# Kernel optimization log

Hardware: AMD Instinct MI355X
Metric: run time of the kernel (lower is better)

The kernel has to match this reference:

```python
import jax, jax.numpy as jnp
import numpy as np

B, V_IN, V_OUT, C_IN, C_OUT, K, NNZ = 16, 1024, 4096, 128, 256, 18, 16384

def setup_inputs() -> dict:
    key = jax.random.key(0)
    ks = jax.random.split(key, 10)
    def lin(k, fan_in, fan_out):
        s = 1.0 / np.sqrt(fan_in)
        return jax.random.normal(k, (fan_in, fan_out), jnp.float32) * s
    return {
        "x": jax.random.normal(ks[0], (B, V_IN, C_IN), jnp.float32),
        "vals": jax.random.uniform(ks[1], (NNZ,), jnp.float32),
        "W1": lin(ks[2], 1 * C_IN, C_OUT),
        "b1": jnp.zeros((C_OUT,), jnp.float32),
        "Wd3": lin(ks[3], (K // 3) * C_IN, C_OUT // 4),
        "bd3": jnp.zeros((C_OUT // 4,), jnp.float32),
        "W2d3": lin(ks[4], (K // 3 * 2) * C_IN, C_OUT // 4),
        "b2d3": jnp.zeros((C_OUT // 4,), jnp.float32),
        "Wf": lin(ks[5], K * C_IN, C_OUT // 2),
        "bf": jnp.zeros((C_OUT // 2,), jnp.float32),
        "rows": jax.random.randint(ks[6], (NNZ,), 0, V_OUT, jnp.int32),
        "cols": jax.random.randint(ks[7], (NNZ,), 0, V_IN, jnp.int32),
        "spiral_idx": jax.random.randint(ks[8], (V_OUT, K), 0, V_OUT, jnp.int32),
    }

def _pool(x, rows, cols, vals, dim_size):
    # sparse upsample: gather cols, scale, scatter-add to rows
    gathered = x[:, cols, :] * vals[None, :, None]  # [B, nnz, C]
    return jnp.zeros((x.shape[0], dim_size, x.shape[2]), x.dtype).at[:, rows, :].add(gathered)

def _spiral_conv(feat, idx, W, b):
    # gather fixed spiral neighborhoods then shared linear layer
    Bz, V, C = feat.shape[0], idx.shape[0], feat.shape[2]
    g = feat[:, idx.reshape(-1), :].reshape(Bz, V, idx.shape[1] * C)  # [B, V, K*C]
    return g @ W + b

def reference(x, vals, W1, b1, Wd3, bd3, W2d3, b2d3, Wf, bf, rows, cols, spiral_idx):
    out = _pool(x, rows, cols, vals, V_OUT)  # [B, V_OUT, C_IN]
    k = spiral_idx.shape[1]
    short_cut = _spiral_conv(out, spiral_idx[:, :1], W1, b1)
    p_d3 = _spiral_conv(out, spiral_idx[:, : k // 3], Wd3, bd3)
    p_2d3 = _spiral_conv(out, spiral_idx[:, : k // 3 * 2], W2d3, b2d3)
    p = _spiral_conv(out, spiral_idx, Wf, bf)
    f = jnp.concatenate((p, p_2d3, p_d3), axis=2)  # [B, V_OUT, C_OUT]
    return jax.nn.relu(short_cut + f)
```

## Files before the change

### kernel.cpp

```cpp
#include <hip/hip_runtime.h>
#include <hip/hip_bf16.h>

#define B_SZ   16
#define V_IN   1024
#define V_OUT  4096
#define C_IN   128
#define C_OUT  256
#define K_NB   18
#define NNZ    16384
#define K_GEMM (K_NB * C_IN)
#define BK     64
#define NKT    (K_GEMM / BK)

typedef __attribute__((ext_vector_type(8))) short bf16x8;
typedef __attribute__((ext_vector_type(4))) float f32x4;

#define GLOAD16(src, dst) __builtin_amdgcn_global_load_lds( \
    (const __attribute__((address_space(1))) unsigned int*)(src), \
    (__attribute__((address_space(3))) unsigned int*)(dst), 16, 0, 0)

#define MFMA16(a_, b_, c_) __builtin_amdgcn_mfma_f32_16x16x32_bf16((a_), (b_), (c_), 0, 0, 0)

__global__ __launch_bounds__(1024) void csr_kernel(const int* __restrict__ rows,
                                                   int* __restrict__ offsets,
                                                   int* __restrict__ perm) {
    __shared__ int cnt[V_OUT];
    __shared__ int wsum[16];
    const int t = threadIdx.x;
    const int lane = t & 63, wid = t >> 6;
#pragma unroll
    for (int i = t; i < V_OUT; i += 1024) cnt[i] = 0;
    __syncthreads();
#pragma unroll
    for (int n = t; n < NNZ; n += 1024) atomicAdd(&cnt[rows[n]], 1);
    __syncthreads();
    const int base4 = t * 4;
    int c0 = cnt[base4], c1 = cnt[base4 + 1], c2 = cnt[base4 + 2], c3 = cnt[base4 + 3];
    int tot = c0 + c1 + c2 + c3;
    int v = tot;
#pragma unroll
    for (int d = 1; d < 64; d <<= 1) {
        int u = __shfl_up(v, d);
        if (lane >= d) v += u;
    }
    if (lane == 63) wsum[wid] = v;
    __syncthreads();
    int wbase = 0;
#pragma unroll
    for (int w = 0; w < 16; ++w) wbase += (w < wid) ? wsum[w] : 0;
    int incl = wbase + v;
    int excl = incl - tot;
    offsets[base4]     = excl;
    offsets[base4 + 1] = excl + c0;
    offsets[base4 + 2] = excl + c0 + c1;
    offsets[base4 + 3] = excl + c0 + c1 + c2;
    if (t == 1023) offsets[V_OUT] = incl;
    __syncthreads();
    cnt[base4]     = excl;
    cnt[base4 + 1] = excl + c0;
    cnt[base4 + 2] = excl + c0 + c1;
    cnt[base4 + 3] = excl + c0 + c1 + c2;
    __syncthreads();
#pragma unroll
    for (int n = t; n < NNZ; n += 1024) {
        int pos = atomicAdd(&cnt[rows[n]], 1);
        perm[pos] = n;
    }
}

__global__ __launch_bounds__(512) void pool_kernel(
    const float* __restrict__ x, const float* __restrict__ vals,
    const int* __restrict__ cols, const int* __restrict__ offsets,
    const int* __restrict__ perm, __hip_bfloat16* __restrict__ pool) {
    int r = blockIdx.x;
    int t = threadIdx.x;
    int b = t >> 5, c4 = t & 31;
    int j0 = offsets[r], j1 = offsets[r + 1];
    const float4* xb = (const float4*)x + (size_t)b * (V_IN * 32);
    float4 acc = {0.f, 0.f, 0.f, 0.f};
    for (int j = j0; j < j1; ++j) {
        int n = perm[j];
        float v = vals[n];
        float4 xv = xb[cols[n] * 32 + c4];
        acc.x += v * xv.x; acc.y += v * xv.y; acc.z += v * xv.z; acc.w += v * xv.w;
    }
    ushort4 o;
    o.x = __builtin_bit_cast(unsigned short, __float2bfloat16(acc.x));
    o.y = __builtin_bit_cast(unsigned short, __float2bfloat16(acc.y));
    o.z = __builtin_bit_cast(unsigned short, __float2bfloat16(acc.z));
    o.w = __builtin_bit_cast(unsigned short, __float2bfloat16(acc.w));
    ((ushort4*)pool)[((size_t)b * V_OUT + r) * 32 + c4] = o;
}

__global__ __launch_bounds__(256) void wcomb_kernel(
    const float* __restrict__ W1, const float* __restrict__ Wd3,
    const float* __restrict__ W2d3, const float* __restrict__ Wf,
    const float* __restrict__ b1, const float* __restrict__ bd3,
    const float* __restrict__ b2d3, const float* __restrict__ bf,
    __hip_bfloat16* __restrict__ wTs, float* __restrict__ bias) {
    const int blk = blockIdx.x;
    const int t   = threadIdx.x;
    if (blk == NKT * 4) {
        float v = b1[t];
        if (t < 128)      v += bf[t];
        else if (t < 192) v += b2d3[t - 128];
        else              v += bd3[t - 192];
        bias[t] = v;
        return;
    }
    const int kt = blk >> 2, part = blk & 3;
    __shared__ __hip_bfloat16 img[4096];
    const int k0 = kt * 64;

    auto put = [&](int cl, int col7, int kl, float v) {
        int kb    = (kl >> 3) << 4;
        int kslot = kb ^ (col7 << 4);
        int idx   = (((cl << 3) | (kslot >> 4)) << 3) | (kl & 7);
        img[idx] = __float2bfloat16(v);
    };

    if (part < 2) {
        const int cbase = part << 6;
        for (int i = t; i < 4096; i += 256) {
            int kl = i >> 6, cl = i & 63;
            int col = cbase + cl, r = k0 + kl;
            float v = Wf[r * 128 + col];
            if (r < 128) v += W1[r * 256 + col];
            put(cl, col & 7, kl, v);
        }
    } else if (part == 2) {
        for (int i = t; i < 4096; i += 256) {
            int kl = i >> 6, cl = i & 63;
            int r = k0 + kl;
            float v = (r < 1536) ? W2d3[r * 64 + cl] : 0.f;
            if (r < 128) v += W1[r * 256 + 128 + cl];
            put(cl, cl & 7, kl, v);
        }
    } else {
        for (int i = t; i < 4096; i += 256) {
            int kl = i >> 6, cl = i & 63;
            int r = k0 + kl;
            float v = (r < 768) ? Wd3[r * 64 + cl] : 0.f;
            if (r < 128) v += W1[r * 256 + 192 + cl];
            put(cl, cl & 7, kl, v);
        }
    }
    __syncthreads();
    ulonglong2* dst = (ulonglong2*)(wTs + (size_t)kt * 16384 + part * 4096);
    const ulonglong2* srcv = (const ulonglong2*)img;
#pragma unroll
    for (int i = t; i < 512; i += 256) dst[i] = srcv[i];
}

__global__ __launch_bounds__(1024, 4) void gemm_kernel(
    const __hip_bfloat16* __restrict__ pool,
    const __hip_bfloat16* __restrict__ wTs,
    const float* __restrict__ bias,
    const int* __restrict__ spiral,
    float* __restrict__ out)
{
    __shared__ __align__(16) char smem[149504];
    int* spl = (int*)(smem + 131072);

    const int tid  = threadIdx.x;
    const int lane = tid & 63;
    const int wid  = tid >> 6;
    const int wc   = wid & 3;
    const int wm   = (wid >> 2) << 6;

    const int bid = blockIdx.x;
    const int bm  = ((bid & 7) << 5) + (bid >> 3);
    const int b   = bm >> 4;
    const int v0  = (bm & 15) << 8;

    for (int i = tid; i < 256 * K_NB; i += 1024) {
        int j = i >> 8, row = i & 255;
        spl[i] = spiral[(v0 + row) * K_NB + j];
    }
    asm volatile("s_waitcnt vmcnt(0) lgkmcnt(0)" ::: "memory");
    __builtin_amdgcn_s_barrier();

    const char* poolBytes = (const char*)(pool + (size_t)b * V_OUT * C_IN);
    const char* wTsBytes  = (const char*)wTs;
    const int sb = ((tid & 7) << 4) ^ (((tid >> 3) & 7) << 4);

    auto stageA = [&](int kt) {
        const int j   = kt >> 1;
        const int c0b = (kt & 1) << 7;
        char* dst = smem + ((kt & 1) << 15);
#pragma unroll
        for (int ch = 0; ch < 2; ++ch) {
            int flat = (ch << 10) + tid;
            int sidx = spl[(j << 8) + (flat >> 3)];
            GLOAD16(poolBytes + ((size_t)sidx << 8) + (c0b + sb), dst + flat * 16);
        }
    };
    auto stageB = [&](int kt) {
        const char* src = wTsBytes + ((size_t)kt << 15);
        char* dst = smem + 65536 + ((kt & 1) << 15);
#pragma unroll
        for (int ch = 0; ch < 2; ++ch) {
            int off = ((ch << 10) + tid) << 4;
            GLOAD16(src + off, dst + off);
        }
    };

    const int l15   = lane & 15;
    const int swm   = (lane & 7) << 4;
    const int klane = (lane >> 4) << 4;
    const int aBase = (wm + l15) << 7;
    const int bOff0 = (((2 * wc)     << 4) + l15) << 7;
    const int bOff1 = (((2 * wc + 1) << 4) + l15) << 7;
    const int bOff2 = (((8 + wc)     << 4) + l15) << 7;
    const int bOff3 = (((12 + wc)    << 4) + l15) << 7;

    f32x4 acc[4][4] = {};

    stageA(0);
    stageB(0);

    for (int kt = 0; kt < NKT; ++kt) {
        const int s = kt & 1;
        const char* As = smem + (s << 15);
        const char* Bs = smem + 65536 + (s << 15);

        if (kt + 1 < NKT) {
            stageA(kt + 1);
            stageB(kt + 1);
            asm volatile("s_waitcnt vmcnt(4)" ::: "memory");
        } else {
            asm volatile("s_waitcnt vmcnt(0)" ::: "memory");
        }
        __builtin_amdgcn_s_barrier();
        __builtin_amdgcn_sched_barrier(0);

        const bool doMid   = kt < 24;
        const bool doShort = kt < 12;

#pragma unroll
        for (int ks = 0; ks < 2; ++ks) {
            const int kk = (ks * 64 + klane) ^ swm;
            bf16x8 a0 = *(const bf16x8*)(As + aBase + (0 << 11) + kk);
            bf16x8 a1 = *(const bf16x8*)(As + aBase + (1 << 11) + kk);
            bf16x8 a2 = *(const bf16x8*)(As + aBase + (2 << 11) + kk);
            bf16x8 a3 = *(const bf16x8*)(As + aBase + (3 << 11) + kk);
            bf16x8 bb0 = *(const bf16x8*)(Bs + bOff0 + kk);
            bf16x8 bb1 = *(const bf16x8*)(Bs + bOff1 + kk);
            __builtin_amdgcn_s_setprio(1);
            acc[0][0] = MFMA16(a0, bb0, acc[0][0]);
            acc[1][0] = MFMA16(a1, bb0, acc[1][0]);
            acc[2][0] = MFMA16(a2, bb0, acc[2][0]);
            acc[3][0] = MFMA16(a3, bb0, acc[3][0]);
            acc[0][1] = MFMA16(a0, bb1, acc[0][1]);
            acc[1][1] = MFMA16(a1, bb1, acc[1][1]);
            acc[2][1] = MFMA16(a2, bb1, acc[2][1]);
            acc[3][1] = MFMA16(a3, bb1, acc[3][1]);
            __builtin_amdgcn_s_setprio(0);
            if (doMid) {
                bf16x8 bb2 = *(const bf16x8*)(Bs + bOff2 + kk);
                __builtin_amdgcn_s_setprio(1);
                acc[0][2] = MFMA16(a0, bb2, acc[0][2]);
                acc[1][2] = MFMA16(a1, bb2, acc[1][2]);
                acc[2][2] = MFMA16(a2, bb2, acc[2][2]);
                acc[3][2] = MFMA16(a3, bb2, acc[3][2]);
                __builtin_amdgcn_s_setprio(0);
            }
            if (doShort) {
                bf16x8 bb3 = *(const bf16x8*)(Bs + bOff3 + kk);
                __builtin_amdgcn_s_setprio(1);
                acc[0][3] = MFMA16(a0, bb3, acc[0][3]);
                acc[1][3] = MFMA16(a1, bb3, acc[1][3]);
                acc[2][3] = MFMA16(a2, bb3, acc[2][3]);
                acc[3][3] = MFMA16(a3, bb3, acc[3][3]);
                __builtin_amdgcn_s_setprio(0);
            }
        }

        __builtin_amdgcn_s_barrier();
        __builtin_amdgcn_sched_barrier(0);
    }

    const int nt[4] = {2 * wc, 2 * wc + 1, 8 + wc, 12 + wc};
#pragma unroll
    for (int ni = 0; ni < 4; ++ni) {
        int col = (nt[ni] << 4) + l15;
        float bz = bias[col];
#pragma unroll
        for (int mi = 0; mi < 4; ++mi) {
            int row0 = v0 + wm + mi * 16 + ((lane >> 4) << 2);
#pragma unroll
            for (int r4 = 0; r4 < 4; ++r4) {
                float v = acc[mi][ni][r4] + bz;
                out[((size_t)(b * V_OUT + row0 + r4)) * C_OUT + col] = v > 0.f ? v : 0.f;
            }
        }
    }
}

extern "C" void kernel_launch(void* const* d_in, const int* in_sizes, int n_in,
                              void* d_out, int out_size, void* d_ws, size_t ws_size,
                              hipStream_t stream) {
    const float* x     = (const float*)d_in[0];
    const float* vals  = (const float*)d_in[1];
    const float* W1    = (const float*)d_in[2];
    const float* b1    = (const float*)d_in[3];
    const float* Wd3   = (const float*)d_in[4];
    const float* bd3   = (const float*)d_in[5];
    const float* W2d3  = (const float*)d_in[6];
    const float* b2d3  = (const float*)d_in[7];
    const float* Wf    = (const float*)d_in[8];
    const float* bf    = (const float*)d_in[9];
    const int*   rows  = (const int*)d_in[10];
    const int*   cols  = (const int*)d_in[11];
    const int*   spiral= (const int*)d_in[12];
    float* out = (float*)d_out;

    char* ws = (char*)d_ws;
    __hip_bfloat16* pool = (__hip_bfloat16*)ws;
    __hip_bfloat16* wTs  = (__hip_bfloat16*)(ws + 16777216);
    float* bias          = (float*)(ws + 16777216 + 1179648);
    int*   offsets       = (int*)(ws + 16777216 + 1179648 + 1024);
    int*   perm          = offsets + V_OUT + 4;

    csr_kernel<<<1, 1024, 0, stream>>>(rows, offsets, perm);
    pool_kernel<<<V_OUT, 512, 0, stream>>>(x, vals, cols, offsets, perm, pool);
    wcomb_kernel<<<NKT * 4 + 1, 256, 0, stream>>>(W1, Wd3, W2d3, Wf, b1, bd3, b2d3, bf, wTs, bias);
    gemm_kernel<<<256, 1024, 0, stream>>>(pool, wTs, bias, spiral, out);
}
```

Before: 114.9 us.

## Split CSR build into multi-block kernels and defer weight staging in GEMM

The single-block CSR construction becomes a memset, a multi-block histogram kernel with global atomics, a single-block scan and a multi-block fill kernel, so the serial one-block setup parallelises across the GPU. The GEMM now copies spiral indices contiguously into shared memory, transposing the read pattern when staging A. It also issues the next B tile load after the first k-substep instead of before the wait, so the wait only covers A loads. This adds three extra launches plus a memset, and the later B prefetch shortens the time left to hide its latency.

```diff
diff --git a/kernel.cpp b/kernel.cpp
--- a/kernel.cpp
+++ b/kernel.cpp
@@ -21,21 +21,17 @@
 
 #define MFMA16(a_, b_, c_) __builtin_amdgcn_mfma_f32_16x16x32_bf16((a_), (b_), (c_), 0, 0, 0)
 
-__global__ __launch_bounds__(1024) void csr_kernel(const int* __restrict__ rows,
-                                                   int* __restrict__ offsets,
-                                                   int* __restrict__ perm) {
-    __shared__ int cnt[V_OUT];
+__global__ void hist_kernel(const int* __restrict__ rows, int* counts) {
+    int n = blockIdx.x * blockDim.x + threadIdx.x;
+    if (n < NNZ) atomicAdd(&counts[rows[n]], 1);
+}
+
+__global__ void scan_kernel(const int* __restrict__ counts, int* offsets, int* cursor) {
     __shared__ int wsum[16];
-    const int t = threadIdx.x;
-    const int lane = t & 63, wid = t >> 6;
-#pragma unroll
-    for (int i = t; i < V_OUT; i += 1024) cnt[i] = 0;
-    __syncthreads();
-#pragma unroll
-    for (int n = t; n < NNZ; n += 1024) atomicAdd(&cnt[rows[n]], 1);
-    __syncthreads();
-    const int base4 = t * 4;
-    int c0 = cnt[base4], c1 = cnt[base4 + 1], c2 = cnt[base4 + 2], c3 = cnt[base4 + 3];
+    int t = threadIdx.x;
+    int lane = t & 63, wid = t >> 6;
+    int base4 = t * 4;
+    int c0 = counts[base4], c1 = counts[base4 + 1], c2 = counts[base4 + 2], c3 = counts[base4 + 3];
     int tot = c0 + c1 + c2 + c3;
     int v = tot;
 #pragma unroll
@@ -54,16 +50,18 @@
     offsets[base4 + 1] = excl + c0;
     offsets[base4 + 2] = excl + c0 + c1;
     offsets[base4 + 3] = excl + c0 + c1 + c2;
+    cursor[base4]     = excl;
+    cursor[base4 + 1] = excl + c0;
+    cursor[base4 + 2] = excl + c0 + c1;
+    cursor[base4 + 3] = excl + c0 + c1 + c2;
     if (t == 1023) offsets[V_OUT] = incl;
-    __syncthreads();
-    cnt[base4]     = excl;
-    cnt[base4 + 1] = excl + c0;
-    cnt[base4 + 2] = excl + c0 + c1;
-    cnt[base4 + 3] = excl + c0 + c1 + c2;
-    __syncthreads();
-#pragma unroll
-    for (int n = t; n < NNZ; n += 1024) {
-        int pos = atomicAdd(&cnt[rows[n]], 1);
+}
+
+__global__ void fill_kernel(const int* __restrict__ rows, int* cursor, int* perm) {
+    int n = blockIdx.x * blockDim.x + threadIdx.x;
+    if (n < NNZ) {
+        int r = rows[n];
+        int pos = atomicAdd(&cursor[r], 1);
         perm[pos] = n;
     }
 }
@@ -173,10 +171,7 @@
     const int b   = bm >> 4;
     const int v0  = (bm & 15) << 8;
 
-    for (int i = tid; i < 256 * K_NB; i += 1024) {
-        int j = i >> 8, row = i & 255;
-        spl[i] = spiral[(v0 + row) * K_NB + j];
-    }
+    for (int i = tid; i < 256 * K_NB; i += 1024) spl[i] = spiral[v0 * K_NB + i];
     asm volatile("s_waitcnt vmcnt(0) lgkmcnt(0)" ::: "memory");
     __builtin_amdgcn_s_barrier();
 
@@ -191,7 +186,7 @@
 #pragma unroll
         for (int ch = 0; ch < 2; ++ch) {
             int flat = (ch << 10) + tid;
-            int sidx = spl[(j << 8) + (flat >> 3)];
+            int sidx = spl[(flat >> 3) * K_NB + j];
             GLOAD16(poolBytes + ((size_t)sidx << 8) + (c0b + sb), dst + flat * 16);
         }
     };
@@ -226,8 +221,7 @@
 
         if (kt + 1 < NKT) {
             stageA(kt + 1);
-            stageB(kt + 1);
-            asm volatile("s_waitcnt vmcnt(4)" ::: "memory");
+            asm volatile("s_waitcnt vmcnt(2)" ::: "memory");
         } else {
             asm volatile("s_waitcnt vmcnt(0)" ::: "memory");
         }
@@ -274,6 +268,7 @@
                 acc[3][3] = MFMA16(a3, bb3, acc[3][3]);
                 __builtin_amdgcn_s_setprio(0);
             }
+            if (ks == 0 && kt + 1 < NKT) stageB(kt + 1);
         }
 
         __builtin_amdgcn_s_barrier();
@@ -319,10 +314,15 @@
     __hip_bfloat16* pool = (__hip_bfloat16*)ws;
     __hip_bfloat16* wTs  = (__hip_bfloat16*)(ws + 16777216);
     float* bias          = (float*)(ws + 16777216 + 1179648);
-    int*   offsets       = (int*)(ws + 16777216 + 1179648 + 1024);
-    int*   perm          = offsets + V_OUT + 4;
-
-    csr_kernel<<<1, 1024, 0, stream>>>(rows, offsets, perm);
+    int*   counts        = (int*)(ws + 16777216 + 1179648 + 1024);
+    int*   offsets       = counts + V_OUT;
+    int*   cursor        = offsets + V_OUT + 4;
+    int*   perm          = cursor + V_OUT;
+
+    hipMemsetAsync(counts, 0, V_OUT * sizeof(int), stream);
+    hist_kernel<<<NNZ / 256, 256, 0, stream>>>(rows, counts);
+    scan_kernel<<<1, 1024, 0, stream>>>(counts, offsets, cursor);
+    fill_kernel<<<NNZ / 256, 256, 0, stream>>>(rows, cursor, perm);
     pool_kernel<<<V_OUT, 512, 0, stream>>>(x, vals, cols, offsets, perm, pool);
     wcomb_kernel<<<NKT * 4 + 1, 256, 0, stream>>>(W1, Wd3, W2d3, Wf, b1, bd3, b2d3, bf, wTs, bias);
     gemm_kernel<<<256, 1024, 0, stream>>>(pool, wTs, bias, spiral, out);
```

Result: faster. 107.1 us (-6.8%).
